# Kernel tuning notes

Hardware: AMD Instinct MI355X
Metric: run time of the kernel (lower is better)

Reference implementation:

```python
import jax, jax.numpy as jnp
import numpy as np

B, S, H2 = 32, 4096, 512  # H2 = 2*hidden_size


def setup_inputs() -> dict:
    key = jax.random.key(0)
    ks = jax.random.split(key, 10)
    s = 1.0 / np.sqrt(H2)
    return {
        "decoder_state": jax.random.normal(ks[0], (B, 1, H2), jnp.float32),
        "encoder_outputs": jax.random.normal(ks[1], (B, S, H2), jnp.float32),
        "coverage_vector": jax.random.uniform(ks[2], (B, S, H2), jnp.float32),
        "W_h": jax.random.uniform(ks[3], (H2, H2), jnp.float32, -s, s),
        "b_h": jax.random.uniform(ks[4], (H2,), jnp.float32, -s, s),
        "W_s": jax.random.uniform(ks[5], (H2, H2), jnp.float32, -s, s),
        "b_s": jax.random.uniform(ks[6], (H2,), jnp.float32, -s, s),
        "W_c": jax.random.uniform(ks[7], (H2, H2), jnp.float32, -s, s),
        "b_c": jax.random.uniform(ks[8], (H2,), jnp.float32, -s, s),
        "v": jax.random.uniform(ks[9], (H2, 1), jnp.float32, -s, s),
    }


def reference(decoder_state, encoder_outputs, coverage_vector,
              W_h, b_h, W_s, b_s, W_c, b_c, v):
    # additive attention features: [B, S, 2H]
    e = jnp.tanh(encoder_outputs @ W_h + b_h
                 + decoder_state @ W_s + b_s      # broadcasts over S
                 + coverage_vector @ W_c + b_c)
    scores = e @ v                                # [B, S, 1]
    attn_dist = jax.nn.softmax(scores, axis=1)    # softmax over source positions
    # weighted sum of encoder outputs: [B, 1, 2H]
    h_star_t = jnp.einsum('bsi,bsd->bid', attn_dist, encoder_outputs)
    coverage_new = coverage_vector + attn_dist    # broadcast over feature dim
    return h_star_t, attn_dist, coverage_new
```

## Files before the change

### kernel.cpp

```cpp
#include <hip/hip_runtime.h>
#include <hip/hip_bf16.h>
#include <stdint.h>

#define H2    512
#define BATCH 32
#define SEQ   4096
#define BM    64
#define NPER  16

typedef __attribute__((ext_vector_type(4))) float f32x4;
typedef __attribute__((ext_vector_type(8))) short bf16x8;

__device__ __forceinline__ unsigned short f2bf(float f) {
    union { float f; unsigned u; } v; v.f = f;
    unsigned r = v.u + 0x7FFF + ((v.u >> 16) & 1);
    return (unsigned short)(r >> 16);
}

__device__ __forceinline__ uint4 cvt8_bf16(f32x4 lo, f32x4 hi) {
    uint4 r;
    asm("v_cvt_pk_bf16_f32 %0, %1, %2" : "=v"(r.x) : "v"(lo[0]), "v"(lo[1]));
    asm("v_cvt_pk_bf16_f32 %0, %1, %2" : "=v"(r.y) : "v"(lo[2]), "v"(lo[3]));
    asm("v_cvt_pk_bf16_f32 %0, %1, %2" : "=v"(r.z) : "v"(hi[0]), "v"(hi[1]));
    asm("v_cvt_pk_bf16_f32 %0, %1, %2" : "=v"(r.w) : "v"(hi[2]), "v"(hi[3]));
    return r;
}

__device__ __forceinline__ float fast_tanh(float x) {
    float e = __builtin_amdgcn_exp2f(x * 2.88539008177793f);
    return 1.0f - 2.0f * __builtin_amdgcn_rcpf(e + 1.0f);
}

__global__ void kprep_w(const float* __restrict__ Wh, const float* __restrict__ Wc,
                        unsigned short* __restrict__ wt) {
    int c    = blockIdx.x * blockDim.x + threadIdx.x;
    int lane = c & 63;
    int cb   = (c >> 6) & 31;
    int kt   = c >> 11;
    int col  = cb * 16 + (lane & 15);
    int k0   = kt * 32 + (lane >> 4) * 8;
    unsigned short tmp[8];
#pragma unroll
    for (int j = 0; j < 8; ++j) {
        int kg = k0 + j;
        float w = (kg < 512) ? Wh[kg * 512 + col] : Wc[(kg - 512) * 512 + col];
        tmp[j] = f2bf(w);
    }
    *reinterpret_cast<uint4*>(wt + (size_t)c * 8) = *reinterpret_cast<const uint4*>(tmp);
}

__global__ void kprep_q(const float* __restrict__ dec, const float* __restrict__ Ws,
                        const float* __restrict__ bh, const float* __restrict__ bs,
                        const float* __restrict__ bc, float* __restrict__ q) {
    __shared__ float dsh[512];
    int b = blockIdx.x, t = threadIdx.x;
    dsh[t]       = dec[b * 512 + t];
    dsh[t + 256] = dec[b * 512 + 256 + t];
    __syncthreads();
    float a0 = 0.f, a1 = 0.f;
#pragma unroll 4
    for (int k = 0; k < 512; ++k) {
        float d = dsh[k];
        a0 = fmaf(d, Ws[k * 512 + t], a0);
        a1 = fmaf(d, Ws[k * 512 + 256 + t], a1);
    }
    q[b * 512 + t]       = a0 + bh[t] + bs[t] + bc[t];
    q[b * 512 + 256 + t] = a1 + bh[256 + t] + bs[256 + t] + bc[256 + t];
}

__launch_bounds__(512, 4)
__global__ void kgemm(const float* __restrict__ enc, const float* __restrict__ cov,
                      const unsigned short* __restrict__ wt,
                      const float* __restrict__ q, const float* __restrict__ vvec,
                      float* __restrict__ wout, float* __restrict__ hpart,
                      float* __restrict__ Zpart) {
    __shared__ unsigned short Asm[2][4096];
    __shared__ float qv[H2];
    __shared__ float vv[H2];
    __shared__ float sred[BM][8];
    __shared__ float wsh[BM];

    int tid  = threadIdx.x;
    int lane = tid & 63, wn = tid >> 6;

    int cpx  = gridDim.x >> 3;
    int swz  = (blockIdx.x & 7) * cpx + (blockIdx.x >> 3);
    int row0 = swz * BM;
    int b    = row0 >> 12;

    qv[tid] = q[b * H2 + tid];
    vv[tid] = vvec[tid];

    int r = tid >> 3, k8 = tid & 7;
    const float* aeb = enc + (size_t)(row0 + r) * H2 + k8 * 8;
    const float* acb = cov + (size_t)(row0 + r) * H2 + k8 * 8;
    unsigned awb = (unsigned)((k8 >> 2) * 4096 + (r >> 4) * 1024 + (k8 & 3) * 256 +
                              (((r & 15) * 16) ^ ((k8 & 3) << 4)));
    unsigned arb = (unsigned)((lane >> 4) * 256 +
                              (((lane & 15) * 16) ^ ((lane >> 4) << 4)));
    const bf16x8* bb = reinterpret_cast<const bf16x8*>(wt) +
                       (size_t)(wn * 4) * 64 + lane;

    f32x4  acc[4][4] = {};
    bf16x8 bfr[4], af[4];
    f32x4  pA[2][2];

#define SB0 __builtin_amdgcn_sched_barrier(0);
#define A_PTR(T) ((((T) < 8) ? aeb : acb) + ((T) & 7) * 64)
#define DS_AF(CUR, S)                                                          \
    _Pragma("unroll")                                                          \
    for (int mi = 0; mi < 4; ++mi)                                             \
        af[mi] = *reinterpret_cast<const bf16x8*>(                             \
            (char*)Asm[CUR] + (S) * 4096 + mi * 1024 + arb);
#define LOAD_B(KT32)                                                           \
    _Pragma("unroll")                                                          \
    for (int ni = 0; ni < 4; ++ni)                                             \
        bfr[ni] = bb[(size_t)(KT32) * 2048 + ni * 64];
#define MFMA16                                                                 \
    __builtin_amdgcn_s_setprio(1);                                             \
    _Pragma("unroll")                                                          \
    for (int mi = 0; mi < 4; ++mi)                                             \
        _Pragma("unroll")                                                      \
        for (int ni = 0; ni < 4; ++ni)                                         \
            acc[mi][ni] = __builtin_amdgcn_mfma_f32_16x16x32_bf16(             \
                af[mi], bfr[ni], acc[mi][ni], 0, 0, 0);                        \
    __builtin_amdgcn_s_setprio(0);

#define BODY(T, CUR, PC, DO_PN, DO_B0, DO_STAGE)                               \
  {                                                                            \
    DS_AF(CUR, 0)                                                              \
    SB0                                                                        \
    MFMA16                                  \
    SB0                                                                        \
    LOAD_B((T) * 2 + 1)                            \
    DS_AF(CUR, 1)                                                              \
    if (DO_PN) {                                                               \
        const float* _p = A_PTR((T) + 2);                                      \
        pA[(PC) ^ 1][0] = *reinterpret_cast<const f32x4*>(_p);                 \
        pA[(PC) ^ 1][1] = *reinterpret_cast<const f32x4*>(_p + 4);             \
    }                                                                          \
    SB0                                                                        \
    MFMA16                   \
    SB0                                                                        \
    if (DO_B0) { LOAD_B((T) * 2 + 2) }          \
    if (DO_STAGE) {                                                            \
        uint4 _u = cvt8_bf16(pA[PC][0], pA[PC][1]);                            \
        *reinterpret_cast<uint4*>((char*)Asm[(CUR) ^ 1] + awb) = _u;           \
    }                                                                          \
    asm volatile("s_waitcnt lgkmcnt(0)" ::: "memory");                         \
    SB0                                                                        \
    __builtin_amdgcn_s_barrier();                                              \
    SB0                                                                        \
  }

    LOAD_B(0)
    {
        f32x4 a0 = *reinterpret_cast<const f32x4*>(aeb);
        f32x4 a1 = *reinterpret_cast<const f32x4*>(aeb + 4);
        pA[1][0] = *reinterpret_cast<const f32x4*>(aeb + 64);
        pA[1][1] = *reinterpret_cast<const f32x4*>(aeb + 68);
        SB0
        uint4 u = cvt8_bf16(a0, a1);
        *reinterpret_cast<uint4*>((char*)Asm[0] + awb) = u;
    }
    asm volatile("s_waitcnt lgkmcnt(0)" ::: "memory");
    SB0
    __builtin_amdgcn_s_barrier();
    SB0

#pragma unroll 1
    for (int p = 0; p < 7; ++p) {
        const int t0 = p * 2;
        BODY(t0,     0, 1, true, true, true)
        BODY(t0 + 1, 1, 0, true, true, true)
    }
    BODY(14, 0, 1, false, true,  true)
    BODY(15, 1, 0, false, false, false)

#undef SB0
#undef A_PTR
#undef DS_AF
#undef LOAD_B
#undef MFMA16
#undef BODY

    float ps[4][4] = {};
#pragma unroll
    for (int mi = 0; mi < 4; ++mi)
#pragma unroll
        for (int ni = 0; ni < 4; ++ni) {
            int colg = wn * 64 + ni * 16 + (lane & 15);
            float qq = qv[colg], vl = vv[colg];
#pragma unroll
            for (int j = 0; j < 4; ++j) {
                float e = fast_tanh(acc[mi][ni][j] + qq);
                ps[mi][j] = fmaf(e, vl, ps[mi][j]);
            }
        }
#pragma unroll
    for (int mi = 0; mi < 4; ++mi)
#pragma unroll
        for (int j = 0; j < 4; ++j) {
            float s = ps[mi][j];
            s += __shfl_xor(s, 1);
            s += __shfl_xor(s, 2);
            s += __shfl_xor(s, 4);
            s += __shfl_xor(s, 8);
            if ((lane & 15) == 0)
                sred[mi * 16 + (lane >> 4) * 4 + j][wn] = s;
        }
    __syncthreads();

    if (tid < BM) {
        float s = 0.f;
#pragma unroll
        for (int w = 0; w < 8; ++w) s += sred[tid][w];
        float wv = __builtin_amdgcn_exp2f((s - 16.0f) * 1.4426950408889634f);
        wsh[tid] = wv;
        wout[row0 + tid] = wv;
        float zs = wv;
#pragma unroll
        for (int o = 1; o < 64; o <<= 1) zs += __shfl_xor(zs, o);
        if (tid == 0) Zpart[swz] = zs;
    }
    __syncthreads();

    {
        const float* eb = enc + (size_t)row0 * H2 + tid;
        float h0 = 0.f, h1 = 0.f, h2 = 0.f, h3 = 0.f;
#pragma unroll 4
        for (int rr = 0; rr < BM; rr += 4) {
            h0 = fmaf(wsh[rr + 0], eb[(size_t)(rr + 0) * H2], h0);
            h1 = fmaf(wsh[rr + 1], eb[(size_t)(rr + 1) * H2], h1);
            h2 = fmaf(wsh[rr + 2], eb[(size_t)(rr + 2) * H2], h2);
            h3 = fmaf(wsh[rr + 3], eb[(size_t)(rr + 3) * H2], h3);
        }
        hpart[(size_t)swz * H2 + tid] = (h0 + h1) + (h2 + h3);
    }
}

__global__ void knorm(const float* __restrict__ hpart, const float* __restrict__ Zpart,
                      float* __restrict__ Zb, float* __restrict__ out) {
    __shared__ float zsh;
    int b = blockIdx.x, t = threadIdx.x;
    if (t == 0) {
        float z = 0.f;
#pragma unroll 8
        for (int i = 0; i < 64; ++i) z += Zpart[b * 64 + i];
        zsh = z;
        Zb[b] = z;
    }
    float h = 0.f;
    const float* hp = hpart + (size_t)b * 64 * H2 + t;
#pragma unroll 8
    for (int i = 0; i < 64; ++i) h += hp[(size_t)i * H2];
    __syncthreads();
    out[b * H2 + t] = h / zsh;
}

__global__ void kcov2(const float* __restrict__ cov, const float* __restrict__ w,
                      const float* __restrict__ Zb, float* __restrict__ out) {
    float* attn = out + 16384;
    float* covn = out + 16384 + 131072;
    int blk = blockIdx.x;
    int b = blk >> 6, ck = blk & 63;
    int s0 = ck * 64;
    int t  = threadIdx.x;
    int f4 = (t & 127) * 4;
    int rp = t >> 7;
    float rZ = 1.0f / Zb[b];
    size_t base = (size_t)b * SEQ * H2;
#pragma unroll 2
    for (int i = 0; i < 32; ++i) {
        int s = s0 + i * 2 + rp;
        float a = w[b * 4096 + s] * rZ;
        size_t idx = base + (size_t)s * H2 + f4;
        f32x4 c4 = *reinterpret_cast<const f32x4*>(cov + idx);
        c4 += a;
        __builtin_nontemporal_store(c4, reinterpret_cast<f32x4*>(covn + idx));
        if (f4 == 0) attn[b * 4096 + s] = a;
    }
}

extern "C" void kernel_launch(void* const* d_in, const int* in_sizes, int n_in,
                              void* d_out, int out_size, void* d_ws, size_t ws_size,
                              hipStream_t stream) {
    const float* dec = (const float*)d_in[0];
    const float* enc = (const float*)d_in[1];
    const float* cov = (const float*)d_in[2];
    const float* Wh  = (const float*)d_in[3];
    const float* bh  = (const float*)d_in[4];
    const float* Ws  = (const float*)d_in[5];
    const float* bs  = (const float*)d_in[6];
    const float* Wc  = (const float*)d_in[7];
    const float* bc  = (const float*)d_in[8];
    const float* v   = (const float*)d_in[9];
    float* out = (float*)d_out;

    char* ws = (char*)d_ws;
    unsigned short* wt = (unsigned short*)ws;
    float* q     = (float*)(ws + 0x100000);
    float* wbuf  = (float*)(ws + 0x110000);
    float* hpart = (float*)(ws + 0x190000);
    float* Zpart = (float*)(ws + 0x590000);
    float* Zb    = (float*)(ws + 0x592000);

    kprep_w <<<dim3(256),  dim3(256),  0, stream>>>(Wh, Wc, wt);
    kprep_q <<<dim3(32),   dim3(256),  0, stream>>>(dec, Ws, bh, bs, bc, q);
    kgemm   <<<dim3(2048), dim3(512),  0, stream>>>(enc, cov, wt, q, v,
                                                    wbuf, hpart, Zpart);
    knorm   <<<dim3(32),   dim3(512),  0, stream>>>(hpart, Zpart, Zb, out);
    kcov2   <<<dim3(2048), dim3(256),  0, stream>>>(cov, wbuf, Zb, out);
}
```

Baseline: 367.7 us.

## Load A fragments directly from global into registers, drop LDS staging, enlarge tile

The GEMM kernel no longer stages the fp32 encoder/coverage tile through shared memory as bf16. Each wave now loads its A fragments straight from global memory into registers and converts them in place. Block rows grow to 128 with a 2x4 wave grid covering 64x128 per wave, and the grid is halved with launch bounds relaxed to 2 blocks per CU. The goal is to remove the LDS round trip and the per-step barriers, at the cost of losing A-tile sharing across the four column waves (each A row is fetched by four waves) and using more registers. Zpart and hpart become 32 partials per batch, so the reduction kernel is adjusted to match.

```diff
diff --git a/kernel.cpp b/kernel.cpp
--- a/kernel.cpp
+++ b/kernel.cpp
@@ -5,8 +5,8 @@
 #define H2    512
 #define BATCH 32
 #define SEQ   4096
-#define BM    64
-#define NPER  16
+#define BM    128
+#define NT32  32
 
 typedef __attribute__((ext_vector_type(4))) float f32x4;
 typedef __attribute__((ext_vector_type(8))) short bf16x8;
@@ -17,13 +17,13 @@
     return (unsigned short)(r >> 16);
 }
 
-__device__ __forceinline__ uint4 cvt8_bf16(f32x4 lo, f32x4 hi) {
-    uint4 r;
-    asm("v_cvt_pk_bf16_f32 %0, %1, %2" : "=v"(r.x) : "v"(lo[0]), "v"(lo[1]));
-    asm("v_cvt_pk_bf16_f32 %0, %1, %2" : "=v"(r.y) : "v"(lo[2]), "v"(lo[3]));
-    asm("v_cvt_pk_bf16_f32 %0, %1, %2" : "=v"(r.z) : "v"(hi[0]), "v"(hi[1]));
-    asm("v_cvt_pk_bf16_f32 %0, %1, %2" : "=v"(r.w) : "v"(hi[2]), "v"(hi[3]));
-    return r;
+__device__ __forceinline__ bf16x8 cvt8(f32x4 lo, f32x4 hi) {
+    union { uint4 u; bf16x8 h; } r;
+    asm("v_cvt_pk_bf16_f32 %0, %1, %2" : "=v"(r.u.x) : "v"(lo[0]), "v"(lo[1]));
+    asm("v_cvt_pk_bf16_f32 %0, %1, %2" : "=v"(r.u.y) : "v"(lo[2]), "v"(lo[3]));
+    asm("v_cvt_pk_bf16_f32 %0, %1, %2" : "=v"(r.u.z) : "v"(hi[0]), "v"(hi[1]));
+    asm("v_cvt_pk_bf16_f32 %0, %1, %2" : "=v"(r.u.w) : "v"(hi[2]), "v"(hi[3]));
+    return r.h;
 }
 
 __device__ __forceinline__ float fast_tanh(float x) {
@@ -68,20 +68,20 @@
     q[b * 512 + 256 + t] = a1 + bh[256 + t] + bs[256 + t] + bc[256 + t];
 }
 
-__launch_bounds__(512, 4)
+__launch_bounds__(512, 2)
 __global__ void kgemm(const float* __restrict__ enc, const float* __restrict__ cov,
                       const unsigned short* __restrict__ wt,
                       const float* __restrict__ q, const float* __restrict__ vvec,
                       float* __restrict__ wout, float* __restrict__ hpart,
                       float* __restrict__ Zpart) {
-    __shared__ unsigned short Asm[2][4096];
     __shared__ float qv[H2];
     __shared__ float vv[H2];
-    __shared__ float sred[BM][8];
+    __shared__ float sred[BM][4];
     __shared__ float wsh[BM];
 
     int tid  = threadIdx.x;
-    int lane = tid & 63, wn = tid >> 6;
+    int lane = tid & 63, wid = tid >> 6;
+    int wm   = wid >> 2, wn = wid & 3;
 
     int cpx  = gridDim.x >> 3;
     int swz  = (blockIdx.x & 7) * cpx + (blockIdx.x >> 3);
@@ -91,105 +91,70 @@
     qv[tid] = q[b * H2 + tid];
     vv[tid] = vvec[tid];
 
-    int r = tid >> 3, k8 = tid & 7;
-    const float* aeb = enc + (size_t)(row0 + r) * H2 + k8 * 8;
-    const float* acb = cov + (size_t)(row0 + r) * H2 + k8 * 8;
-    unsigned awb = (unsigned)((k8 >> 2) * 4096 + (r >> 4) * 1024 + (k8 & 3) * 256 +
-                              (((r & 15) * 16) ^ ((k8 & 3) << 4)));
-    unsigned arb = (unsigned)((lane >> 4) * 256 +
-                              (((lane & 15) * 16) ^ ((lane >> 4) << 4)));
+    const float* ap0 = enc + (size_t)(row0 + wm * 64 + (lane & 15)) * H2 +
+                       ((lane >> 4) << 3);
+    const float* cp0 = cov + (size_t)(row0 + wm * 64 + (lane & 15)) * H2 +
+                       ((lane >> 4) << 3);
     const bf16x8* bb = reinterpret_cast<const bf16x8*>(wt) +
-                       (size_t)(wn * 4) * 64 + lane;
-
-    f32x4  acc[4][4] = {};
-    bf16x8 bfr[4], af[4];
-    f32x4  pA[2][2];
+                       (size_t)(wn * 8) * 64 + lane;
+
+    f32x4  acc[4][8] = {};
+    f32x4  pa[4][2];
+    bf16x8 bf[8];
 
 #define SB0 __builtin_amdgcn_sched_barrier(0);
-#define A_PTR(T) ((((T) < 8) ? aeb : acb) + ((T) & 7) * 64)
-#define DS_AF(CUR, S)                                                          \
+#define ISSUE_PA(T)                                                            \
+    {                                                                          \
+        const float* _base = ((T) < 16) ? ap0 : cp0;                           \
+        const int _off = (((T) & 15) << 5);                                    \
+        _Pragma("unroll")                                                      \
+        for (int mi = 0; mi < 4; ++mi) {                                       \
+            const float* _p = _base + (size_t)mi * (16 * H2) + _off;           \
+            pa[mi][0] = *reinterpret_cast<const f32x4*>(_p);                   \
+            pa[mi][1] = *reinterpret_cast<const f32x4*>(_p + 4);               \
+        }                                                                      \
+    }
+#define ISSUE_BF(T)                                                            \
     _Pragma("unroll")                                                          \
-    for (int mi = 0; mi < 4; ++mi)                                             \
-        af[mi] = *reinterpret_cast<const bf16x8*>(                             \
-            (char*)Asm[CUR] + (S) * 4096 + mi * 1024 + arb);
-#define LOAD_B(KT32)                                                           \
-    _Pragma("unroll")                                                          \
-    for (int ni = 0; ni < 4; ++ni)                                             \
-        bfr[ni] = bb[(size_t)(KT32) * 2048 + ni * 64];
-#define MFMA16                                                                 \
-    __builtin_amdgcn_s_setprio(1);                                             \
-    _Pragma("unroll")                                                          \
-    for (int mi = 0; mi < 4; ++mi)                                             \
-        _Pragma("unroll")                                                      \
-        for (int ni = 0; ni < 4; ++ni)                                         \
-            acc[mi][ni] = __builtin_amdgcn_mfma_f32_16x16x32_bf16(             \
-                af[mi], bfr[ni], acc[mi][ni], 0, 0, 0);                        \
-    __builtin_amdgcn_s_setprio(0);
-
-#define BODY(T, CUR, PC, DO_PN, DO_B0, DO_STAGE)                               \
-  {                                                                            \
-    DS_AF(CUR, 0)                                                              \
-    SB0                                                                        \
-    MFMA16                                  \
-    SB0                                                                        \
-    LOAD_B((T) * 2 + 1)                            \
-    DS_AF(CUR, 1)                                                              \
-    if (DO_PN) {                                                               \
-        const float* _p = A_PTR((T) + 2);                                      \
-        pA[(PC) ^ 1][0] = *reinterpret_cast<const f32x4*>(_p);                 \
-        pA[(PC) ^ 1][1] = *reinterpret_cast<const f32x4*>(_p + 4);             \
-    }                                                                          \
-    SB0                                                                        \
-    MFMA16                   \
-    SB0                                                                        \
-    if (DO_B0) { LOAD_B((T) * 2 + 2) }          \
-    if (DO_STAGE) {                                                            \
-        uint4 _u = cvt8_bf16(pA[PC][0], pA[PC][1]);                            \
-        *reinterpret_cast<uint4*>((char*)Asm[(CUR) ^ 1] + awb) = _u;           \
-    }                                                                          \
-    asm volatile("s_waitcnt lgkmcnt(0)" ::: "memory");                         \
-    SB0                                                                        \
-    __builtin_amdgcn_s_barrier();                                              \
-    SB0                                                                        \
-  }
-
-    LOAD_B(0)
-    {
-        f32x4 a0 = *reinterpret_cast<const f32x4*>(aeb);
-        f32x4 a1 = *reinterpret_cast<const f32x4*>(aeb + 4);
-        pA[1][0] = *reinterpret_cast<const f32x4*>(aeb + 64);
-        pA[1][1] = *reinterpret_cast<const f32x4*>(aeb + 68);
-        SB0
-        uint4 u = cvt8_bf16(a0, a1);
-        *reinterpret_cast<uint4*>((char*)Asm[0] + awb) = u;
-    }
-    asm volatile("s_waitcnt lgkmcnt(0)" ::: "memory");
+    for (int ni = 0; ni < 8; ++ni)                                             \
+        bf[ni] = bb[(size_t)(T) * 2048 + ni * 64];
+
+    ISSUE_PA(0)
+    ISSUE_BF(0)
     SB0
-    __builtin_amdgcn_s_barrier();
-    SB0
-
-#pragma unroll 1
-    for (int p = 0; p < 7; ++p) {
-        const int t0 = p * 2;
-        BODY(t0,     0, 1, true, true, true)
-        BODY(t0 + 1, 1, 0, true, true, true)
-    }
-    BODY(14, 0, 1, false, true,  true)
-    BODY(15, 1, 0, false, false, false)
-
+
+#pragma unroll 2
+    for (int t = 0; t < NT32; ++t) {
+        bf16x8 af[4];
+#pragma unroll
+        for (int mi = 0; mi < 4; ++mi)
+            af[mi] = cvt8(pa[mi][0], pa[mi][1]);
+        SB0
+        if (t + 1 < NT32) { ISSUE_PA(t + 1) }
+        SB0
+        __builtin_amdgcn_s_setprio(1);
+#pragma unroll
+        for (int mi = 0; mi < 4; ++mi)
+#pragma unroll
+            for (int ni = 0; ni < 8; ++ni)
+                acc[mi][ni] = __builtin_amdgcn_mfma_f32_16x16x32_bf16(
+                    af[mi], bf[ni], acc[mi][ni], 0, 0, 0);
+        __builtin_amdgcn_s_setprio(0);
+        SB0
+        if (t + 1 < NT32) { ISSUE_BF(t + 1) }
+        SB0
+    }
 #undef SB0
-#undef A_PTR
-#undef DS_AF
-#undef LOAD_B
-#undef MFMA16
-#undef BODY
-
+#undef ISSUE_PA
+#undef ISSUE_BF
+
+    __syncthreads();
     float ps[4][4] = {};
 #pragma unroll
     for (int mi = 0; mi < 4; ++mi)
 #pragma unroll
-        for (int ni = 0; ni < 4; ++ni) {
-            int colg = wn * 64 + ni * 16 + (lane & 15);
+        for (int ni = 0; ni < 8; ++ni) {
+            int colg = wn * 128 + ni * 16 + (lane & 15);
             float qq = qv[colg], vl = vv[colg];
 #pragma unroll
             for (int j = 0; j < 4; ++j) {
@@ -207,23 +172,22 @@
             s += __shfl_xor(s, 4);
             s += __shfl_xor(s, 8);
             if ((lane & 15) == 0)
-                sred[mi * 16 + (lane >> 4) * 4 + j][wn] = s;
+                sred[wm * 64 + mi * 16 + (lane >> 4) * 4 + j][wn] = s;
         }
     __syncthreads();
 
     if (tid < BM) {
-        float s = 0.f;
-#pragma unroll
-        for (int w = 0; w < 8; ++w) s += sred[tid][w];
+        float s = sred[tid][0] + sred[tid][1] + sred[tid][2] + sred[tid][3];
         float wv = __builtin_amdgcn_exp2f((s - 16.0f) * 1.4426950408889634f);
         wsh[tid] = wv;
         wout[row0 + tid] = wv;
         float zs = wv;
 #pragma unroll
         for (int o = 1; o < 64; o <<= 1) zs += __shfl_xor(zs, o);
-        if (tid == 0) Zpart[swz] = zs;
-    }
-    __syncthreads();
+        if ((tid & 63) == 0) sred[0][tid >> 6] = zs;
+    }
+    __syncthreads();
+    if (tid == 0) Zpart[swz] = sred[0][0] + sred[0][1];
 
     {
         const float* eb = enc + (size_t)row0 * H2 + tid;
@@ -246,14 +210,14 @@
     if (t == 0) {
         float z = 0.f;
 #pragma unroll 8
-        for (int i = 0; i < 64; ++i) z += Zpart[b * 64 + i];
+        for (int i = 0; i < 32; ++i) z += Zpart[b * 32 + i];
         zsh = z;
         Zb[b] = z;
     }
     float h = 0.f;
-    const float* hp = hpart + (size_t)b * 64 * H2 + t;
+    const float* hp = hpart + (size_t)b * 32 * H2 + t;
 #pragma unroll 8
-    for (int i = 0; i < 64; ++i) h += hp[(size_t)i * H2];
+    for (int i = 0; i < 32; ++i) h += hp[(size_t)i * H2];
     __syncthreads();
     out[b * H2 + t] = h / zsh;
 }
@@ -307,7 +271,7 @@
 
     kprep_w <<<dim3(256),  dim3(256),  0, stream>>>(Wh, Wc, wt);
     kprep_q <<<dim3(32),   dim3(256),  0, stream>>>(dec, Ws, bh, bs, bc, q);
-    kgemm   <<<dim3(2048), dim3(512),  0, stream>>>(enc, cov, wt, q, v,
+    kgemm   <<<dim3(1024), dim3(512),  0, stream>>>(enc, cov, wt, q, v,
                                                     wbuf, hpart, Zpart);
     knorm   <<<dim3(32),   dim3(512),  0, stream>>>(hpart, Zpart, Zb, out);
     kcov2   <<<dim3(2048), dim3(256),  0, stream>>>(cov, wbuf, Zb, out);
```

Result: slower. 527.5 us (+43.5%).

## Double GEMM row tile and stage weight fragments into LDS via global_load_lds

Applied to the files above, without the earlier changes.

Raises the row tile from 64 to 128 with a 2x4 wave grid, so each block computes a 128x512 tile and half as many blocks are launched. The bf16 weight slices are now brought into double-buffered LDS with direct global-to-LDS loads instead of being read from global memory into registers by every wave. The pipeline is rebuilt around this with vmcnt waits and barriers, using 80KB of dynamic LDS. This is meant to cut repeated weight traffic and raise reuse per block, at the cost of more accumulator registers, lower occupancy (launch bounds drop to 2 blocks) and extra barriers per k-step.

```diff
diff --git a/kernel.cpp b/kernel.cpp
--- a/kernel.cpp
+++ b/kernel.cpp
@@ -5,11 +5,14 @@
 #define H2    512
 #define BATCH 32
 #define SEQ   4096
-#define BM    64
-#define NPER  16
+#define BM    128
+#define NT32  32
 
 typedef __attribute__((ext_vector_type(4))) float f32x4;
 typedef __attribute__((ext_vector_type(8))) short bf16x8;
+
+typedef __attribute__((address_space(3))) unsigned int       as3_uint;
+typedef const __attribute__((address_space(1))) unsigned int as1_uint;
 
 __device__ __forceinline__ unsigned short f2bf(float f) {
     union { float f; unsigned u; } v; v.f = f;
@@ -17,7 +20,7 @@
     return (unsigned short)(r >> 16);
 }
 
-__device__ __forceinline__ uint4 cvt8_bf16(f32x4 lo, f32x4 hi) {
+__device__ __forceinline__ uint4 cvt8(f32x4 lo, f32x4 hi) {
     uint4 r;
     asm("v_cvt_pk_bf16_f32 %0, %1, %2" : "=v"(r.x) : "v"(lo[0]), "v"(lo[1]));
     asm("v_cvt_pk_bf16_f32 %0, %1, %2" : "=v"(r.y) : "v"(lo[2]), "v"(lo[3]));
@@ -68,128 +71,141 @@
     q[b * 512 + 256 + t] = a1 + bh[256 + t] + bs[256 + t] + bc[256 + t];
 }
 
-__launch_bounds__(512, 4)
+__launch_bounds__(512, 2)
 __global__ void kgemm(const float* __restrict__ enc, const float* __restrict__ cov,
                       const unsigned short* __restrict__ wt,
                       const float* __restrict__ q, const float* __restrict__ vvec,
                       float* __restrict__ wout, float* __restrict__ hpart,
                       float* __restrict__ Zpart) {
-    __shared__ unsigned short Asm[2][4096];
-    __shared__ float qv[H2];
-    __shared__ float vv[H2];
-    __shared__ float sred[BM][8];
-    __shared__ float wsh[BM];
+    extern __shared__ char lds[];
+    char* AsmB = lds + 65536;
 
     int tid  = threadIdx.x;
-    int lane = tid & 63, wn = tid >> 6;
+    int lane = tid & 63, wid = tid >> 6;
+    int wm   = wid >> 2, wn = wid & 3;
 
     int cpx  = gridDim.x >> 3;
     int swz  = (blockIdx.x & 7) * cpx + (blockIdx.x >> 3);
     int row0 = swz * BM;
     int b    = row0 >> 12;
 
-    qv[tid] = q[b * H2 + tid];
-    vv[tid] = vvec[tid];
-
-    int r = tid >> 3, k8 = tid & 7;
-    const float* aeb = enc + (size_t)(row0 + r) * H2 + k8 * 8;
-    const float* acb = cov + (size_t)(row0 + r) * H2 + k8 * 8;
-    unsigned awb = (unsigned)((k8 >> 2) * 4096 + (r >> 4) * 1024 + (k8 & 3) * 256 +
-                              (((r & 15) * 16) ^ ((k8 & 3) << 4)));
+    int ar = tid >> 2, ako = tid & 3;
+    const float* aeb = enc + (size_t)(row0 + ar) * H2 + ako * 8;
+    const float* acb = cov + (size_t)(row0 + ar) * H2 + ako * 8;
+    unsigned awb = (unsigned)((ar >> 4) * 1024 + ako * 256 +
+                              (((ar & 15) * 16) ^ (ako << 4)));
     unsigned arb = (unsigned)((lane >> 4) * 256 +
                               (((lane & 15) * 16) ^ ((lane >> 4) << 4)));
-    const bf16x8* bb = reinterpret_cast<const bf16x8*>(wt) +
-                       (size_t)(wn * 4) * 64 + lane;
-
-    f32x4  acc[4][4] = {};
-    bf16x8 bfr[4], af[4];
-    f32x4  pA[2][2];
+
+    f32x4 acc[4][8] = {};
+    f32x4 pA[2][2];
 
 #define SB0 __builtin_amdgcn_sched_barrier(0);
-#define A_PTR(T) ((((T) < 8) ? aeb : acb) + ((T) & 7) * 64)
-#define DS_AF(CUR, S)                                                          \
+#define A_SRC(T) (((T) < 16) ? (aeb + (T) * 32) : (acb + ((T) - 16) * 32))
+#define GLL1(T, BUF, I)                                                        \
+    __builtin_amdgcn_global_load_lds(                                          \
+        (as1_uint*)(wt + ((size_t)(T) * 32 + wid * 4 + (I)) * 512 + lane * 8), \
+        (as3_uint*)(lds + (BUF) * 32768 + (wid * 4 + (I)) * 1024), 16, 0, 0);
+#define DS_AF(CUR)                                                             \
     _Pragma("unroll")                                                          \
     for (int mi = 0; mi < 4; ++mi)                                             \
         af[mi] = *reinterpret_cast<const bf16x8*>(                             \
-            (char*)Asm[CUR] + (S) * 4096 + mi * 1024 + arb);
-#define LOAD_B(KT32)                                                           \
+            AsmB + (CUR) * 8192 + (wm * 4 + mi) * 1024 + arb);
+#define DS_BF(CUR, H)                                                          \
     _Pragma("unroll")                                                          \
     for (int ni = 0; ni < 4; ++ni)                                             \
-        bfr[ni] = bb[(size_t)(KT32) * 2048 + ni * 64];
-#define MFMA16                                                                 \
+        bf[ni] = *reinterpret_cast<const bf16x8*>(                             \
+            lds + (CUR) * 32768 + (wn * 8 + (H) * 4 + ni) * 1024 + lane * 16);
+#define MFMA16(H)                                                              \
     __builtin_amdgcn_s_setprio(1);                                             \
     _Pragma("unroll")                                                          \
     for (int mi = 0; mi < 4; ++mi)                                             \
         _Pragma("unroll")                                                      \
         for (int ni = 0; ni < 4; ++ni)                                         \
-            acc[mi][ni] = __builtin_amdgcn_mfma_f32_16x16x32_bf16(             \
-                af[mi], bfr[ni], acc[mi][ni], 0, 0, 0);                        \
+            acc[mi][(H) * 4 + ni] = __builtin_amdgcn_mfma_f32_16x16x32_bf16(   \
+                af[mi], bf[ni], acc[mi][(H) * 4 + ni], 0, 0, 0);               \
     __builtin_amdgcn_s_setprio(0);
-
-#define BODY(T, CUR, PC, DO_PN, DO_B0, DO_STAGE)                               \
+#define LGKM0 asm volatile("s_waitcnt lgkmcnt(0)" ::: "memory"); SB0
+
+#define BODY(T, CUR, NXT, PC, VMC, DO_B, DO_A2, DO_CVT)                        \
   {                                                                            \
-    DS_AF(CUR, 0)                                                              \
-    SB0                                                                        \
-    MFMA16                                  \
-    SB0                                                                        \
-    LOAD_B((T) * 2 + 1)                            \
-    DS_AF(CUR, 1)                                                              \
-    if (DO_PN) {                                                               \
-        const float* _p = A_PTR((T) + 2);                                      \
-        pA[(PC) ^ 1][0] = *reinterpret_cast<const f32x4*>(_p);                 \
-        pA[(PC) ^ 1][1] = *reinterpret_cast<const f32x4*>(_p + 4);             \
+    asm volatile("s_waitcnt vmcnt(" #VMC ")" ::: "memory");                    \
+    SB0                                                                        \
+    __builtin_amdgcn_s_barrier();                                              \
+    SB0                                                                        \
+    bf16x8 af[4], bf[4];                                                       \
+    DS_AF(CUR)                                                                 \
+    DS_BF(CUR, 0)                                                              \
+    if (DO_B) { GLL1((T) + 1, NXT, 0) GLL1((T) + 1, NXT, 1) }                  \
+    if (DO_A2) {                                                               \
+        pA[(PC) ^ 1][0] = *reinterpret_cast<const f32x4*>(A_SRC((T) + 2));     \
     }                                                                          \
     SB0                                                                        \
-    MFMA16                   \
-    SB0                                                                        \
-    if (DO_B0) { LOAD_B((T) * 2 + 2) }          \
-    if (DO_STAGE) {                                                            \
-        uint4 _u = cvt8_bf16(pA[PC][0], pA[PC][1]);                            \
-        *reinterpret_cast<uint4*>((char*)Asm[(CUR) ^ 1] + awb) = _u;           \
+    LGKM0                                                                      \
+    MFMA16(0)                                                                  \
+    SB0                                                                        \
+    __builtin_amdgcn_s_barrier();                                              \
+    SB0                                                                        \
+    DS_BF(CUR, 1)                                                              \
+    if (DO_B) { GLL1((T) + 1, NXT, 2) GLL1((T) + 1, NXT, 3) }                  \
+    if (DO_A2) {                                                               \
+        pA[(PC) ^ 1][1] = *reinterpret_cast<const f32x4*>(A_SRC((T) + 2) + 4); \
     }                                                                          \
-    asm volatile("s_waitcnt lgkmcnt(0)" ::: "memory");                         \
-    SB0                                                                        \
-    __builtin_amdgcn_s_barrier();                                              \
+    if (DO_CVT) {                                                              \
+        uint4 _u = cvt8(pA[PC][0], pA[PC][1]);                                 \
+        *reinterpret_cast<uint4*>(AsmB + (NXT) * 8192 + awb) = _u;             \
+    }                                                                          \
+    SB0                                                                        \
+    LGKM0                                                                      \
+    MFMA16(1)                                                                  \
     SB0                                                                        \
   }
 
-    LOAD_B(0)
+    GLL1(0, 0, 0) GLL1(0, 0, 1) GLL1(0, 0, 2) GLL1(0, 0, 3)
     {
-        f32x4 a0 = *reinterpret_cast<const f32x4*>(aeb);
-        f32x4 a1 = *reinterpret_cast<const f32x4*>(aeb + 4);
-        pA[1][0] = *reinterpret_cast<const f32x4*>(aeb + 64);
-        pA[1][1] = *reinterpret_cast<const f32x4*>(aeb + 68);
+        f32x4 a0 = *reinterpret_cast<const f32x4*>(A_SRC(0));
+        f32x4 a1 = *reinterpret_cast<const f32x4*>(A_SRC(0) + 4);
+        pA[0][0] = *reinterpret_cast<const f32x4*>(A_SRC(1));
+        pA[0][1] = *reinterpret_cast<const f32x4*>(A_SRC(1) + 4);
         SB0
-        uint4 u = cvt8_bf16(a0, a1);
-        *reinterpret_cast<uint4*>((char*)Asm[0] + awb) = u;
-    }
-    asm volatile("s_waitcnt lgkmcnt(0)" ::: "memory");
-    SB0
-    __builtin_amdgcn_s_barrier();
-    SB0
+        uint4 u = cvt8(a0, a1);
+        *reinterpret_cast<uint4*>(AsmB + awb) = u;
+    }
+    LGKM0
 
 #pragma unroll 1
-    for (int p = 0; p < 7; ++p) {
+    for (int p = 0; p < 15; ++p) {
         const int t0 = p * 2;
-        BODY(t0,     0, 1, true, true, true)
-        BODY(t0 + 1, 1, 0, true, true, true)
-    }
-    BODY(14, 0, 1, false, true,  true)
-    BODY(15, 1, 0, false, false, false)
+        BODY(t0,     0, 1, 0, 1, true, true, true)
+        BODY(t0 + 1, 1, 0, 1, 1, true, true, true)
+    }
+    BODY(30, 0, 1, 0, 1, true,  false, true)
+    BODY(31, 1, 0, 1, 0, false, false, false)
 
 #undef SB0
-#undef A_PTR
+#undef A_SRC
+#undef GLL1
 #undef DS_AF
-#undef LOAD_B
+#undef DS_BF
 #undef MFMA16
+#undef LGKM0
 #undef BODY
 
+    float* qv   = (float*)lds;
+    float* vv   = qv + 512;
+    float* sred = vv + 512;
+    float* wsh  = sred + 512;
+    __syncthreads();
+    qv[tid] = q[b * H2 + tid];
+    vv[tid] = vvec[tid];
+    __syncthreads();
+
     float ps[4][4] = {};
 #pragma unroll
     for (int mi = 0; mi < 4; ++mi)
 #pragma unroll
-        for (int ni = 0; ni < 4; ++ni) {
-            int colg = wn * 64 + ni * 16 + (lane & 15);
+        for (int ni = 0; ni < 8; ++ni) {
+            int colg = wn * 128 + ni * 16 + (lane & 15);
             float qq = qv[colg], vl = vv[colg];
 #pragma unroll
             for (int j = 0; j < 4; ++j) {
@@ -207,23 +223,23 @@
             s += __shfl_xor(s, 4);
             s += __shfl_xor(s, 8);
             if ((lane & 15) == 0)
-                sred[mi * 16 + (lane >> 4) * 4 + j][wn] = s;
+                sred[(wm * 64 + mi * 16 + (lane >> 4) * 4 + j) * 4 + wn] = s;
         }
     __syncthreads();
 
     if (tid < BM) {
-        float s = 0.f;
-#pragma unroll
-        for (int w = 0; w < 8; ++w) s += sred[tid][w];
+        float s = sred[tid * 4 + 0] + sred[tid * 4 + 1] +
+                  sred[tid * 4 + 2] + sred[tid * 4 + 3];
         float wv = __builtin_amdgcn_exp2f((s - 16.0f) * 1.4426950408889634f);
         wsh[tid] = wv;
         wout[row0 + tid] = wv;
         float zs = wv;
 #pragma unroll
         for (int o = 1; o < 64; o <<= 1) zs += __shfl_xor(zs, o);
-        if (tid == 0) Zpart[swz] = zs;
-    }
-    __syncthreads();
+        if ((tid & 63) == 0) sred[tid >> 6] = zs;
+    }
+    __syncthreads();
+    if (tid == 0) Zpart[swz] = sred[0] + sred[1];
 
     {
         const float* eb = enc + (size_t)row0 * H2 + tid;
@@ -246,14 +262,14 @@
     if (t == 0) {
         float z = 0.f;
 #pragma unroll 8
-        for (int i = 0; i < 64; ++i) z += Zpart[b * 64 + i];
+        for (int i = 0; i < 32; ++i) z += Zpart[b * 32 + i];
         zsh = z;
         Zb[b] = z;
     }
     float h = 0.f;
-    const float* hp = hpart + (size_t)b * 64 * H2 + t;
+    const float* hp = hpart + (size_t)b * 32 * H2 + t;
 #pragma unroll 8
-    for (int i = 0; i < 64; ++i) h += hp[(size_t)i * H2];
+    for (int i = 0; i < 32; ++i) h += hp[(size_t)i * H2];
     __syncthreads();
     out[b * H2 + t] = h / zsh;
 }
@@ -305,10 +321,17 @@
     float* Zpart = (float*)(ws + 0x590000);
     float* Zb    = (float*)(ws + 0x592000);
 
-    kprep_w <<<dim3(256),  dim3(256),  0, stream>>>(Wh, Wc, wt);
-    kprep_q <<<dim3(32),   dim3(256),  0, stream>>>(dec, Ws, bh, bs, bc, q);
-    kgemm   <<<dim3(2048), dim3(512),  0, stream>>>(enc, cov, wt, q, v,
-                                                    wbuf, hpart, Zpart);
-    knorm   <<<dim3(32),   dim3(512),  0, stream>>>(hpart, Zpart, Zb, out);
-    kcov2   <<<dim3(2048), dim3(256),  0, stream>>>(cov, wbuf, Zb, out);
-}
+    static bool attr_done = false;
+    if (!attr_done) {
+        hipFuncSetAttribute((const void*)kgemm,
+                            hipFuncAttributeMaxDynamicSharedMemorySize, 81920);
+        attr_done = true;
+    }
+
+    kprep_w <<<dim3(256),  dim3(256),  0,     stream>>>(Wh, Wc, wt);
+    kprep_q <<<dim3(32),   dim3(256),  0,     stream>>>(dec, Ws, bh, bs, bc, q);
+    kgemm   <<<dim3(1024), dim3(512),  81920, stream>>>(enc, cov, wt, q, v,
+                                                        wbuf, hpart, Zpart);
+    knorm   <<<dim3(32),   dim3(512),  0,     stream>>>(hpart, Zpart, Zb, out);
+    kcov2   <<<dim3(2048), dim3(256),  0,     stream>>>(cov, wbuf, Zb, out);
+}
```

Measured after the change: 397.8 us. 1.08x slower.
